# Performance work log

Measured on AMD Instinct MI355X. Metric: run time of the kernel, lower is better.

The kernel has to match this reference:

```python
import jax, jax.numpy as jnp
import numpy as np

N = 50000   # num_nodes
E = 640000  # num_edges (avg degree ~12.8)
D = 128     # input_dim
H = 128     # hidden_dim
T = 100     # targets per head


def setup_inputs() -> dict:
    key = jax.random.key(0)
    ks = jax.random.split(key, 20)
    w = lambda k, s: jax.random.normal(k, s, jnp.float32) * 0.02
    return {
        "x": jax.random.normal(ks[0], (N, D), jnp.float32),
        "edge_index": jax.random.randint(ks[1], (2, E), 0, N, dtype=jnp.int32),
        "edge_weight": jax.random.uniform(ks[2], (E,), jnp.float32),
        "ace_idx": jax.random.randint(ks[3], (T,), 0, N, dtype=jnp.int32),
        "h2_idx": jax.random.randint(ks[4], (T,), 0, N, dtype=jnp.int32),
        "W1": w(ks[5], (D, H)), "b1": jnp.zeros((H,), jnp.float32),
        "W2": w(ks[6], (H, H)), "b2": jnp.zeros((H,), jnp.float32),
        "W3": w(ks[7], (H, H)), "b3": jnp.zeros((H,), jnp.float32),
        "Wh": w(ks[8], (H, H)), "bh": jnp.zeros((H,), jnp.float32),
        "Wace": w(ks[9], (H, 1)), "bace": jnp.zeros((1,), jnp.float32),
        "Wh2": w(ks[10], (H, 1)), "bh2": jnp.zeros((1,), jnp.float32),
    }


def gcn_conv(x, src, dst, ew, W, b):
    # PyG GCNConv: add self-loops (weight 1), symmetric D^-1/2 (A+I) D^-1/2, then XW + b
    n = x.shape[0]
    xw = x @ W                                             # [N, H]
    deg = jax.ops.segment_sum(ew, dst, num_segments=n) + 1.0  # +1 from self-loop
    dinv = jax.lax.rsqrt(jnp.maximum(deg, 1e-12))          # deg >= 1 here
    norm = dinv[src] * ew * dinv[dst]                      # per-edge coefficient
    agg = jax.ops.segment_sum(norm[:, None] * xw[src], dst, num_segments=n)
    agg = agg + (dinv * dinv)[:, None] * xw                # self-loop contribution
    return agg + b


def reference(x, edge_index, edge_weight, ace_idx, h2_idx,
              W1, b1, W2, b2, W3, b3, Wh, bh, Wace, bace, Wh2, bh2):
    src, dst = edge_index[0], edge_index[1]
    h = jax.nn.relu(gcn_conv(x, src, dst, edge_weight, W1, b1))
    h = jax.nn.relu(gcn_conv(h, src, dst, edge_weight, W2, b2))
    h = jax.nn.relu(gcn_conv(h, src, dst, edge_weight, W3, b3))
    # dropout is identity in eval mode
    h = jax.nn.relu(h @ Wh + bh)
    ace_pred = h[ace_idx] @ Wace + bace   # [T, 1]
    h2_pred = h[h2_idx] @ Wh2 + bh2       # [T, 1]
    return jnp.concatenate([ace_pred, h2_pred], axis=0)  # [2T, 1]
```

## Files before the change

### kernel.cpp

```cpp
#include <hip/hip_runtime.h>
#include <math.h>

constexpr int N = 50000;
constexpr int E = 640000;
constexpr int D = 128;
constexpr int T = 100;
constexpr int MAXDEG = 64;
constexpr float SC = 256.0f;
constexpr float SCINV = 1.0f / 256.0f;
constexpr int GB = (N + 127) / 128;
constexpr int EBLK = (E + 255) / 256;
constexpr int ZB = N * 8 / 16 / 256 + 1;
constexpr int WCB = 3 * 16384 / 256;

typedef __attribute__((ext_vector_type(8))) _Float16 half8v;
typedef __attribute__((ext_vector_type(8))) unsigned short ushort8v;
typedef __attribute__((ext_vector_type(4))) float f32x4;

__device__ inline float dinv_of(unsigned int degY) {
  return 1.0f / sqrtf((float)degY * (1.0f / 16777216.0f) + 1.0f);
}


__global__ __launch_bounds__(256) void init_kernel(
    const float* __restrict__ W1, const float* __restrict__ W2,
    const float* __restrict__ W3, uint4* __restrict__ degcnt_v,
    unsigned short* __restrict__ wt0, unsigned short* __restrict__ wt1,
    unsigned short* __restrict__ w3kn) {
  int b = blockIdx.x, tid = threadIdx.x;
  if (b < ZB) {
    int i = b * 256 + tid;
    if (i < N * 8 / 16) degcnt_v[i] = uint4{0, 0, 0, 0};
  } else {
    int idx = (b - ZB) * 256 + tid;
    int layer = idx >> 14;
    int r = idx & 16383;
    if (layer == 0) {
      int n = r >> 7, k = r & 127;
      _Float16 h = (_Float16)(W1[k * D + n] * SC);
      wt0[n * D + k] = *(unsigned short*)&h;
    } else if (layer == 1) {
      int n = r >> 7, k = r & 127;
      _Float16 h = (_Float16)W2[k * D + n];
      wt1[n * D + k] = *(unsigned short*)&h;
    } else {
      int k = r >> 7, n = r & 127;
      _Float16 h = (_Float16)W3[k * D + n];
      w3kn[k * D + n] = *(unsigned short*)&h;
    }
  }
}


__global__ void edge_pass_kernel(const float* __restrict__ ew, const int* __restrict__ src,
                                 const int* __restrict__ dst,
                                 unsigned long long* __restrict__ degcnt,
                                 unsigned int* __restrict__ slot) {
  int e = blockIdx.x * 256 + threadIdx.x;
  if (e < E) {
    float w = ew[e];
    int d = dst[e];
    unsigned int fxdeg = __float2uint_rn(w * 16777216.0f);
    unsigned int fx16 = __float2uint_rn(w * 65536.0f);
    if (fx16 > 65535u) fx16 = 65535u;
    unsigned long long old = atomicAdd(&degcnt[d],
                                       ((unsigned long long)fxdeg << 32) | 1ull);
    unsigned int rank = (unsigned int)(old & 0xffffffffull);
    if (rank < MAXDEG)
      slot[(size_t)d * MAXDEG + rank] = (fx16 << 16) | (unsigned int)src[e];
  }
}


template <bool F32A, bool DINV>
__global__ __launch_bounds__(256) void gemm_nolds_kernel(
    const void* __restrict__ Ain, const unsigned short* __restrict__ Bt,
    const uint2* __restrict__ degcnt, unsigned short* __restrict__ out) {
  const int tid = threadIdx.x;
  const int w = tid >> 6, lane = tid & 63;
  const int q = lane >> 4, n16 = lane & 15;
  const int rbase = w * 32;
  const int row0 = blockIdx.x * 128;

  size_t arow[2];
#pragma unroll
  for (int rt = 0; rt < 2; ++rt) {
    int gr = row0 + rbase + rt * 16 + n16;
    if (gr >= N) gr = N - 1;
    arow[rt] = (size_t)gr * D;
  }
  half8v a[4][2];
#pragma unroll
  for (int kc = 0; kc < 4; ++kc) {
    const int ko = kc * 32 + q * 8;
#pragma unroll
    for (int rt = 0; rt < 2; ++rt) {
      if (F32A) {
        const float* A = (const float*)Ain;
        float4 v0 = *(const float4*)&A[arow[rt] + ko];
        float4 v1 = *(const float4*)&A[arow[rt] + ko + 4];
        half8v h;
        h[0] = (_Float16)v0.x; h[1] = (_Float16)v0.y;
        h[2] = (_Float16)v0.z; h[3] = (_Float16)v0.w;
        h[4] = (_Float16)v1.x; h[5] = (_Float16)v1.y;
        h[6] = (_Float16)v1.z; h[7] = (_Float16)v1.w;
        a[kc][rt] = h;
      } else {
        const unsigned short* A = (const unsigned short*)Ain;
        a[kc][rt] = *(const half8v*)&A[arow[rt] + ko];
      }
    }
  }

  f32x4 acc[2][8] = {};
#pragma unroll
  for (int kc = 0; kc < 4; ++kc) {
    const int ko = kc * 32 + q * 8;
#pragma unroll
    for (int ct = 0; ct < 8; ++ct) {
      int n = ct * 16 + n16;
      half8v b = *(const half8v*)&Bt[n * D + ko];
#pragma unroll
      for (int rt = 0; rt < 2; ++rt) {
        acc[rt][ct] = __builtin_amdgcn_mfma_f32_16x16x32_f16(a[kc][rt], b, acc[rt][ct], 0, 0, 0);
      }
    }
  }

#pragma unroll
  for (int rt = 0; rt < 2; ++rt) {
#pragma unroll
    for (int r = 0; r < 4; ++r) {
      int gr = row0 + rbase + rt * 16 + q * 4 + r;
      if (gr < N) {
        float dv = 1.0f;
        if (DINV) dv = dinv_of(degcnt[gr].y);
#pragma unroll
        for (int ct = 0; ct < 8; ++ct) {
          int col = ct * 16 + n16;
          _Float16 h = (_Float16)(DINV ? acc[rt][ct][r] * dv : acc[rt][ct][r]);
          out[(size_t)gr * D + col] = *(unsigned short*)&h;
        }
      }
    }
  }
}


__global__ __launch_bounds__(256) void agg_kernel(
    const unsigned short* __restrict__ z, const unsigned int* __restrict__ slot,
    const uint2* __restrict__ degcnt, const float* __restrict__ bias,
    unsigned short* __restrict__ oP) {
  int g = (blockIdx.x * 256 + threadIdx.x) >> 4;
  int lane = threadIdx.x & 15;
  const unsigned int* degY = (const unsigned int*)degcnt;

  uint2 pg = degcnt[g];
  int cnt = (int)pg.x; if (cnt > MAXDEG) cnt = MAXDEG;
  float dvg = dinv_of(pg.y);
  half8v xv = *(const half8v*)&z[(size_t)g * D + lane * 8];
  float acc[8];
#pragma unroll
  for (int i = 0; i < 8; ++i) acc[i] = dvg * (float)xv[i];

  const unsigned int* sl = slot + (size_t)g * MAXDEG;
  int k = 0;
  for (; k + 4 <= cnt; k += 4) {
    uint4 p = *(const uint4*)&sl[k];
    float d0 = dinv_of(degY[((p.x & 0xffffu) << 1) + 1]);
    float d1 = dinv_of(degY[((p.y & 0xffffu) << 1) + 1]);
    float d2 = dinv_of(degY[((p.z & 0xffffu) << 1) + 1]);
    float d3 = dinv_of(degY[((p.w & 0xffffu) << 1) + 1]);
    float c0 = (float)(p.x >> 16) * (1.0f / 65536.0f) * d0;
    float c1 = (float)(p.y >> 16) * (1.0f / 65536.0f) * d1;
    float c2 = (float)(p.z >> 16) * (1.0f / 65536.0f) * d2;
    float c3 = (float)(p.w >> 16) * (1.0f / 65536.0f) * d3;
    half8v v0 = *(const half8v*)&z[(size_t)(p.x & 0xffffu) * D + lane * 8];
    half8v v1 = *(const half8v*)&z[(size_t)(p.y & 0xffffu) * D + lane * 8];
    half8v v2 = *(const half8v*)&z[(size_t)(p.z & 0xffffu) * D + lane * 8];
    half8v v3 = *(const half8v*)&z[(size_t)(p.w & 0xffffu) * D + lane * 8];
#pragma unroll
    for (int i = 0; i < 8; ++i) {
      acc[i] = fmaf(c0, (float)v0[i], acc[i]);
      acc[i] = fmaf(c1, (float)v1[i], acc[i]);
      acc[i] = fmaf(c2, (float)v2[i], acc[i]);
      acc[i] = fmaf(c3, (float)v3[i], acc[i]);
    }
  }
  for (; k < cnt; ++k) {
    unsigned int p = sl[k];
    float dsv = dinv_of(degY[((p & 0xffffu) << 1) + 1]);
    float c = (float)(p >> 16) * (1.0f / 65536.0f) * dsv;
    half8v v = *(const half8v*)&z[(size_t)(p & 0xffffu) * D + lane * 8];
#pragma unroll
    for (int i = 0; i < 8; ++i) acc[i] = fmaf(c, (float)v[i], acc[i]);
  }

  half8v hv;
#pragma unroll
  for (int i = 0; i < 8; ++i)
    hv[i] = (_Float16)fmaxf(fmaf(dvg, acc[i], bias[lane * 8 + i] * SC), 0.f);
  *(half8v*)&oP[(size_t)g * D + lane * 8] = hv;
}


__global__ __launch_bounds__(256) void l23_heads_kernel(
    const unsigned short* __restrict__ z2, const unsigned int* __restrict__ slot,
    const uint2* __restrict__ degcnt,
    const float* __restrict__ b2, const float* __restrict__ b3,
    const unsigned short* __restrict__ w3kn,
    const float* __restrict__ Wh, const float* __restrict__ bh,
    const int* __restrict__ ace_idx, const int* __restrict__ h2_idx,
    const float* __restrict__ Wace, const float* __restrict__ bace,
    const float* __restrict__ Wh2, const float* __restrict__ bh2,
    float* __restrict__ out) {
  __shared__ float sacc[16][128];
  __shared__ unsigned short w3l[16384];
  __shared__ float svec[128];
  __shared__ float h3v[128];
  __shared__ float psum[2];
  int t = blockIdx.x;
  int tid = threadIdx.x;
  int node; const float* whead; float bhead;
  if (t < T) { node = ace_idx[t];     whead = Wace; bhead = bace[0]; }
  else       { node = h2_idx[t - T];  whead = Wh2;  bhead = bh2[0]; }

#pragma unroll
  for (int it = 0; it < 8; ++it) {
    int idx = tid + it * 256;
    *(ushort8v*)&w3l[idx * 8] = *(const ushort8v*)&w3kn[idx * 8];
  }

  int grp = tid >> 4, lane = tid & 15;
  float b2l[8];
#pragma unroll
  for (int i = 0; i < 8; ++i) b2l[i] = b2[lane * 8 + i] * SC;

  uint2 pn = degcnt[node];
  int tcnt = (int)pn.x; if (tcnt > MAXDEG) tcnt = MAXDEG;
  float dvn = dinv_of(pn.y);
  const unsigned int* tsl = slot + (size_t)node * MAXDEG;
  int nitems = 1 + tcnt;
  float a[8] = {};
  for (int it = grp; it < nitems; it += 16) {
    int u; float wgt;
    if (it == 0) { u = node; wgt = 1.0f; }
    else {
      unsigned int p = tsl[it - 1];
      wgt = (float)(p >> 16) * (1.0f / 65536.0f);
      u = (int)(p & 0xffffu);
    }
    uint2 pu = degcnt[u];
    float dvu = dinv_of(pu.y);
    int cu = (int)pu.x; if (cu > MAXDEG) cu = MAXDEG;
    half8v xv = *(const half8v*)&z2[(size_t)u * D + lane * 8];
    float r[8];
#pragma unroll
    for (int i = 0; i < 8; ++i) r[i] = (float)xv[i];
    const unsigned int* usl = slot + (size_t)u * MAXDEG;
    int e = 0;
    for (; e + 4 <= cu; e += 4) {
      uint4 p4 = *(const uint4*)&usl[e];
      float c0 = (float)(p4.x >> 16) * (1.0f / 65536.0f);
      float c1 = (float)(p4.y >> 16) * (1.0f / 65536.0f);
      float c2 = (float)(p4.z >> 16) * (1.0f / 65536.0f);
      float c3 = (float)(p4.w >> 16) * (1.0f / 65536.0f);
      half8v v0 = *(const half8v*)&z2[(size_t)(p4.x & 0xffffu) * D + lane * 8];
      half8v v1 = *(const half8v*)&z2[(size_t)(p4.y & 0xffffu) * D + lane * 8];
      half8v v2 = *(const half8v*)&z2[(size_t)(p4.z & 0xffffu) * D + lane * 8];
      half8v v3 = *(const half8v*)&z2[(size_t)(p4.w & 0xffffu) * D + lane * 8];
#pragma unroll
      for (int i = 0; i < 8; ++i) {
        r[i] = fmaf(c0, (float)v0[i], r[i]);
        r[i] = fmaf(c1, (float)v1[i], r[i]);
        r[i] = fmaf(c2, (float)v2[i], r[i]);
        r[i] = fmaf(c3, (float)v3[i], r[i]);
      }
    }
    for (; e < cu; ++e) {
      unsigned int p2 = usl[e];
      float c2 = (float)(p2 >> 16) * (1.0f / 65536.0f);
      half8v v = *(const half8v*)&z2[(size_t)(p2 & 0xffffu) * D + lane * 8];
#pragma unroll
      for (int i = 0; i < 8; ++i) r[i] = fmaf(c2, (float)v[i], r[i]);
    }
#pragma unroll
    for (int i = 0; i < 8; ++i) {
      float h2 = fmaxf(fmaf(dvu, r[i], b2l[i]), 0.f);
      a[i] = fmaf(wgt, dvu * h2, a[i]);
    }
  }
#pragma unroll
  for (int i = 0; i < 8; ++i) sacc[grp][lane * 8 + i] = a[i];
  __syncthreads();

  if (tid < 128) {
    float s = 0.f;
#pragma unroll
    for (int gp = 0; gp < 16; ++gp) s += sacc[gp][tid];
    svec[tid] = s * dvn;
  }
  __syncthreads();

  if (tid < 128) {
    float y = b3[tid] * SC;
#pragma unroll 16
    for (int k = 0; k < 128; ++k) {
      _Float16 wv = *(const _Float16*)&w3l[k * D + tid];
      y = fmaf(svec[k], (float)wv, y);
    }
    h3v[tid] = fmaxf(y, 0.f) * SCINV;
  }
  __syncthreads();

  float v = 0.f;
  if (tid < 128) {
    float acc = bh[tid];
#pragma unroll 16
    for (int k = 0; k < 128; ++k)
      acc = fmaf(h3v[k], Wh[k * D + tid], acc);
    v = fmaxf(acc, 0.f) * whead[tid];
  }
#pragma unroll
  for (int off = 32; off; off >>= 1) v += __shfl_down(v, off, 64);
  if (tid < 128 && (tid & 63) == 0) psum[tid >> 6] = v;
  __syncthreads();
  if (tid == 0) out[t] = psum[0] + psum[1] + bhead;
}


extern "C" void kernel_launch(void* const* d_in, const int* in_sizes, int n_in,
                              void* d_out, int out_size, void* d_ws, size_t ws_size,
                              hipStream_t stream) {
  const float* x    = (const float*)d_in[0];
  const int*   ei   = (const int*)d_in[1];
  const float* ew   = (const float*)d_in[2];
  const int*   ace  = (const int*)d_in[3];
  const int*   h2   = (const int*)d_in[4];
  const float* W1 = (const float*)d_in[5];  const float* b1 = (const float*)d_in[6];
  const float* W2 = (const float*)d_in[7];  const float* b2 = (const float*)d_in[8];
  const float* W3 = (const float*)d_in[9];  const float* b3 = (const float*)d_in[10];
  const float* Wh = (const float*)d_in[11]; const float* bh = (const float*)d_in[12];
  const float* Wace = (const float*)d_in[13]; const float* bace = (const float*)d_in[14];
  const float* Wh2  = (const float*)d_in[15]; const float* bh2  = (const float*)d_in[16];
  const int* src = ei;
  const int* dst = ei + E;

  char* w = (char*)d_ws;
  unsigned long long* degcnt = (unsigned long long*)w;  w += (size_t)N * 8;
  unsigned int* slot = (unsigned int*)w;  w += (size_t)N * MAXDEG * 4;
  unsigned short* wt0 = (unsigned short*)w;  w += 16384 * 2;
  unsigned short* wt1 = (unsigned short*)w;  w += 16384 * 2;
  unsigned short* w3kn = (unsigned short*)w; w += 16384 * 2;
  unsigned short* zbuf = (unsigned short*)w; w += (size_t)N * D * 2;
  unsigned short* P1  = (unsigned short*)w;  w += (size_t)N * D * 2;

  const int AG = N * 16 / 256;

  init_kernel<<<ZB + WCB, 256, 0, stream>>>(W1, W2, W3, (uint4*)degcnt, wt0, wt1, w3kn);
  edge_pass_kernel<<<EBLK, 256, 0, stream>>>(ew, src, dst, degcnt, slot);
  gemm_nolds_kernel<true, false><<<GB, 256, 0, stream>>>(x, wt0, nullptr, zbuf);
  agg_kernel<<<AG, 256, 0, stream>>>(zbuf, slot, (const uint2*)degcnt, b1, P1);
  gemm_nolds_kernel<false, true><<<GB, 256, 0, stream>>>(P1, wt1, (const uint2*)degcnt, zbuf);
  l23_heads_kernel<<<2 * T, 256, 0, stream>>>(zbuf, slot, (const uint2*)degcnt,
                                              b2, b3, w3kn, Wh, bh, ace, h2,
                                              Wace, bace, Wh2, bh2, (float*)d_out);
}
```

Baseline: 216.6 us.

## Fuse edge pass with layer-1 GEMM and split target aggregation across blocks

The edge scatter pass and the first GEMM (x@W1), which are independent, now run in one launch, with different blocks taking different roles, so the two overlap and one launch is saved. The edge pass now handles 4 edges per thread. The layer-2/3 head work is split into a partial kernel with 4 blocks per target (800 blocks instead of 200) that writes partial sums to a workspace buffer, plus a finish kernel that reduces them and applies W3 and the heads. This adds one launch and a small buffer in exchange for more parallelism in the latency-bound target stage.

```diff
diff --git a/kernel.cpp b/kernel.cpp
--- a/kernel.cpp
+++ b/kernel.cpp
@@ -9,7 +9,8 @@
 constexpr float SC = 256.0f;
 constexpr float SCINV = 1.0f / 256.0f;
 constexpr int GB = (N + 127) / 128;
-constexpr int EBLK = (E + 255) / 256;
+constexpr int ESL = E / 4;
+constexpr int EB4 = ESL / 256;
 constexpr int ZB = N * 8 / 16 / 256 + 1;
 constexpr int WCB = 3 * 16384 / 256;
 
@@ -52,29 +53,99 @@
 }
 
 
-__global__ void edge_pass_kernel(const float* __restrict__ ew, const int* __restrict__ src,
-                                 const int* __restrict__ dst,
-                                 unsigned long long* __restrict__ degcnt,
-                                 unsigned int* __restrict__ slot) {
-  int e = blockIdx.x * 256 + threadIdx.x;
-  if (e < E) {
-    float w = ew[e];
-    int d = dst[e];
-    unsigned int fxdeg = __float2uint_rn(w * 16777216.0f);
-    unsigned int fx16 = __float2uint_rn(w * 65536.0f);
-    if (fx16 > 65535u) fx16 = 65535u;
-    unsigned long long old = atomicAdd(&degcnt[d],
-                                       ((unsigned long long)fxdeg << 32) | 1ull);
-    unsigned int rank = (unsigned int)(old & 0xffffffffull);
-    if (rank < MAXDEG)
-      slot[(size_t)d * MAXDEG + rank] = (fx16 << 16) | (unsigned int)src[e];
-  }
-}
-
-
-template <bool F32A, bool DINV>
-__global__ __launch_bounds__(256) void gemm_nolds_kernel(
-    const void* __restrict__ Ain, const unsigned short* __restrict__ Bt,
+__global__ __launch_bounds__(256) void fused_eg1_kernel(
+    const float* __restrict__ ew, const int* __restrict__ src,
+    const int* __restrict__ dst,
+    unsigned long long* __restrict__ degcnt, unsigned int* __restrict__ slot,
+    const float* __restrict__ x, const unsigned short* __restrict__ Bt,
+    unsigned short* __restrict__ z1) {
+  const int b = blockIdx.x;
+  const int tid = threadIdx.x;
+  if (b < EB4) {
+    int gid = b * 256 + tid;
+    float w0 = ew[gid + 0 * ESL], w1 = ew[gid + 1 * ESL];
+    float w2 = ew[gid + 2 * ESL], w3 = ew[gid + 3 * ESL];
+    int d0 = dst[gid + 0 * ESL], d1 = dst[gid + 1 * ESL];
+    int d2 = dst[gid + 2 * ESL], d3 = dst[gid + 3 * ESL];
+    int s0 = src[gid + 0 * ESL], s1 = src[gid + 1 * ESL];
+    int s2 = src[gid + 2 * ESL], s3 = src[gid + 3 * ESL];
+#pragma unroll
+    for (int j = 0; j < 4; ++j) {
+      float w = j == 0 ? w0 : j == 1 ? w1 : j == 2 ? w2 : w3;
+      int d   = j == 0 ? d0 : j == 1 ? d1 : j == 2 ? d2 : d3;
+      int s   = j == 0 ? s0 : j == 1 ? s1 : j == 2 ? s2 : s3;
+      unsigned int fxdeg = __float2uint_rn(w * 16777216.0f);
+      unsigned int fx16 = __float2uint_rn(w * 65536.0f);
+      if (fx16 > 65535u) fx16 = 65535u;
+      unsigned long long old = atomicAdd(&degcnt[d],
+                                         ((unsigned long long)fxdeg << 32) | 1ull);
+      unsigned int rank = (unsigned int)(old & 0xffffffffull);
+      if (rank < MAXDEG)
+        slot[(size_t)d * MAXDEG + rank] = (fx16 << 16) | (unsigned int)s;
+    }
+  } else {
+    const int w = tid >> 6, lane = tid & 63;
+    const int q = lane >> 4, n16 = lane & 15;
+    const int rbase = w * 32;
+    const int row0 = (b - EB4) * 128;
+    size_t arow[2];
+#pragma unroll
+    for (int rt = 0; rt < 2; ++rt) {
+      int gr = row0 + rbase + rt * 16 + n16;
+      if (gr >= N) gr = N - 1;
+      arow[rt] = (size_t)gr * D;
+    }
+    half8v a[4][2];
+#pragma unroll
+    for (int kc = 0; kc < 4; ++kc) {
+      const int ko = kc * 32 + q * 8;
+#pragma unroll
+      for (int rt = 0; rt < 2; ++rt) {
+        float4 v0 = *(const float4*)&x[arow[rt] + ko];
+        float4 v1 = *(const float4*)&x[arow[rt] + ko + 4];
+        half8v h;
+        h[0] = (_Float16)v0.x; h[1] = (_Float16)v0.y;
+        h[2] = (_Float16)v0.z; h[3] = (_Float16)v0.w;
+        h[4] = (_Float16)v1.x; h[5] = (_Float16)v1.y;
+        h[6] = (_Float16)v1.z; h[7] = (_Float16)v1.w;
+        a[kc][rt] = h;
+      }
+    }
+    f32x4 acc[2][8] = {};
+#pragma unroll
+    for (int kc = 0; kc < 4; ++kc) {
+      const int ko = kc * 32 + q * 8;
+#pragma unroll
+      for (int ct = 0; ct < 8; ++ct) {
+        int n = ct * 16 + n16;
+        half8v bb = *(const half8v*)&Bt[n * D + ko];
+#pragma unroll
+        for (int rt = 0; rt < 2; ++rt) {
+          acc[rt][ct] = __builtin_amdgcn_mfma_f32_16x16x32_f16(a[kc][rt], bb, acc[rt][ct], 0, 0, 0);
+        }
+      }
+    }
+#pragma unroll
+    for (int rt = 0; rt < 2; ++rt) {
+#pragma unroll
+      for (int r = 0; r < 4; ++r) {
+        int gr = row0 + rbase + rt * 16 + q * 4 + r;
+        if (gr < N) {
+#pragma unroll
+          for (int ct = 0; ct < 8; ++ct) {
+            int col = ct * 16 + n16;
+            _Float16 h = (_Float16)acc[rt][ct][r];
+            z1[(size_t)gr * D + col] = *(unsigned short*)&h;
+          }
+        }
+      }
+    }
+  }
+}
+
+
+__global__ __launch_bounds__(256) void gemm2_kernel(
+    const unsigned short* __restrict__ A, const unsigned short* __restrict__ Bt,
     const uint2* __restrict__ degcnt, unsigned short* __restrict__ out) {
   const int tid = threadIdx.x;
   const int w = tid >> 6, lane = tid & 63;
@@ -94,24 +165,9 @@
   for (int kc = 0; kc < 4; ++kc) {
     const int ko = kc * 32 + q * 8;
 #pragma unroll
-    for (int rt = 0; rt < 2; ++rt) {
-      if (F32A) {
-        const float* A = (const float*)Ain;
-        float4 v0 = *(const float4*)&A[arow[rt] + ko];
-        float4 v1 = *(const float4*)&A[arow[rt] + ko + 4];
-        half8v h;
-        h[0] = (_Float16)v0.x; h[1] = (_Float16)v0.y;
-        h[2] = (_Float16)v0.z; h[3] = (_Float16)v0.w;
-        h[4] = (_Float16)v1.x; h[5] = (_Float16)v1.y;
-        h[6] = (_Float16)v1.z; h[7] = (_Float16)v1.w;
-        a[kc][rt] = h;
-      } else {
-        const unsigned short* A = (const unsigned short*)Ain;
-        a[kc][rt] = *(const half8v*)&A[arow[rt] + ko];
-      }
-    }
-  }
-
+    for (int rt = 0; rt < 2; ++rt)
+      a[kc][rt] = *(const half8v*)&A[arow[rt] + ko];
+  }
   f32x4 acc[2][8] = {};
 #pragma unroll
   for (int kc = 0; kc < 4; ++kc) {
@@ -126,19 +182,17 @@
       }
     }
   }
-
 #pragma unroll
   for (int rt = 0; rt < 2; ++rt) {
 #pragma unroll
     for (int r = 0; r < 4; ++r) {
       int gr = row0 + rbase + rt * 16 + q * 4 + r;
       if (gr < N) {
-        float dv = 1.0f;
-        if (DINV) dv = dinv_of(degcnt[gr].y);
+        float dv = dinv_of(degcnt[gr].y);
 #pragma unroll
         for (int ct = 0; ct < 8; ++ct) {
           int col = ct * 16 + n16;
-          _Float16 h = (_Float16)(DINV ? acc[rt][ct][r] * dv : acc[rt][ct][r]);
+          _Float16 h = (_Float16)(acc[rt][ct][r] * dv);
           out[(size_t)gr * D + col] = *(unsigned short*)&h;
         }
       }
@@ -204,51 +258,35 @@
 }
 
 
-__global__ __launch_bounds__(256) void l23_heads_kernel(
+__global__ __launch_bounds__(256) void l23_part_kernel(
     const unsigned short* __restrict__ z2, const unsigned int* __restrict__ slot,
-    const uint2* __restrict__ degcnt,
-    const float* __restrict__ b2, const float* __restrict__ b3,
-    const unsigned short* __restrict__ w3kn,
-    const float* __restrict__ Wh, const float* __restrict__ bh,
+    const uint2* __restrict__ degcnt, const float* __restrict__ b2,
     const int* __restrict__ ace_idx, const int* __restrict__ h2_idx,
-    const float* __restrict__ Wace, const float* __restrict__ bace,
-    const float* __restrict__ Wh2, const float* __restrict__ bh2,
-    float* __restrict__ out) {
+    float* __restrict__ pacc) {
   __shared__ float sacc[16][128];
-  __shared__ unsigned short w3l[16384];
-  __shared__ float svec[128];
-  __shared__ float h3v[128];
-  __shared__ float psum[2];
-  int t = blockIdx.x;
+  int b = blockIdx.x;
+  int t = b >> 2, p = b & 3;
   int tid = threadIdx.x;
-  int node; const float* whead; float bhead;
-  if (t < T) { node = ace_idx[t];     whead = Wace; bhead = bace[0]; }
-  else       { node = h2_idx[t - T];  whead = Wh2;  bhead = bh2[0]; }
-
-#pragma unroll
-  for (int it = 0; it < 8; ++it) {
-    int idx = tid + it * 256;
-    *(ushort8v*)&w3l[idx * 8] = *(const ushort8v*)&w3kn[idx * 8];
-  }
+  int node = (t < T) ? ace_idx[t] : h2_idx[t - T];
 
   int grp = tid >> 4, lane = tid & 15;
+  int G = p * 16 + grp;
   float b2l[8];
 #pragma unroll
   for (int i = 0; i < 8; ++i) b2l[i] = b2[lane * 8 + i] * SC;
 
   uint2 pn = degcnt[node];
   int tcnt = (int)pn.x; if (tcnt > MAXDEG) tcnt = MAXDEG;
-  float dvn = dinv_of(pn.y);
   const unsigned int* tsl = slot + (size_t)node * MAXDEG;
   int nitems = 1 + tcnt;
   float a[8] = {};
-  for (int it = grp; it < nitems; it += 16) {
+  for (int it = G; it < nitems; it += 64) {
     int u; float wgt;
     if (it == 0) { u = node; wgt = 1.0f; }
     else {
-      unsigned int p = tsl[it - 1];
-      wgt = (float)(p >> 16) * (1.0f / 65536.0f);
-      u = (int)(p & 0xffffu);
+      unsigned int pk = tsl[it - 1];
+      wgt = (float)(pk >> 16) * (1.0f / 65536.0f);
+      u = (int)(pk & 0xffffu);
     }
     uint2 pu = degcnt[u];
     float dvu = dinv_of(pu.y);
@@ -298,7 +336,38 @@
     float s = 0.f;
 #pragma unroll
     for (int gp = 0; gp < 16; ++gp) s += sacc[gp][tid];
-    svec[tid] = s * dvn;
+    pacc[(size_t)(t * 4 + p) * 128 + tid] = s;
+  }
+}
+
+
+__global__ __launch_bounds__(256) void l23_finish_kernel(
+    const uint2* __restrict__ degcnt, const float* __restrict__ pacc,
+    const float* __restrict__ b3, const unsigned short* __restrict__ w3kn,
+    const float* __restrict__ Wh, const float* __restrict__ bh,
+    const int* __restrict__ ace_idx, const int* __restrict__ h2_idx,
+    const float* __restrict__ Wace, const float* __restrict__ bace,
+    const float* __restrict__ Wh2, const float* __restrict__ bh2,
+    float* __restrict__ out) {
+  __shared__ unsigned short w3l[16384];
+  __shared__ float svec[128];
+  __shared__ float h3v[128];
+  __shared__ float psum[2];
+  int t = blockIdx.x;
+  int tid = threadIdx.x;
+  int node; const float* whead; float bhead;
+  if (t < T) { node = ace_idx[t];     whead = Wace; bhead = bace[0]; }
+  else       { node = h2_idx[t - T];  whead = Wh2;  bhead = bh2[0]; }
+
+#pragma unroll
+  for (int it = 0; it < 8; ++it) {
+    int idx = tid + it * 256;
+    *(ushort8v*)&w3l[idx * 8] = *(const ushort8v*)&w3kn[idx * 8];
+  }
+  if (tid < 128) {
+    const float* pa = &pacc[(size_t)t * 4 * 128];
+    float s = pa[tid] + pa[128 + tid] + pa[256 + tid] + pa[384 + tid];
+    svec[tid] = s * dinv_of(degcnt[node].y);
   }
   __syncthreads();
 
@@ -352,17 +421,19 @@
   unsigned short* wt0 = (unsigned short*)w;  w += 16384 * 2;
   unsigned short* wt1 = (unsigned short*)w;  w += 16384 * 2;
   unsigned short* w3kn = (unsigned short*)w; w += 16384 * 2;
+  float* pacc = (float*)w;                   w += (size_t)2 * T * 4 * 128 * 4;
   unsigned short* zbuf = (unsigned short*)w; w += (size_t)N * D * 2;
   unsigned short* P1  = (unsigned short*)w;  w += (size_t)N * D * 2;
 
   const int AG = N * 16 / 256;
 
   init_kernel<<<ZB + WCB, 256, 0, stream>>>(W1, W2, W3, (uint4*)degcnt, wt0, wt1, w3kn);
-  edge_pass_kernel<<<EBLK, 256, 0, stream>>>(ew, src, dst, degcnt, slot);
-  gemm_nolds_kernel<true, false><<<GB, 256, 0, stream>>>(x, wt0, nullptr, zbuf);
+  fused_eg1_kernel<<<EB4 + GB, 256, 0, stream>>>(ew, src, dst, degcnt, slot, x, wt0, zbuf);
   agg_kernel<<<AG, 256, 0, stream>>>(zbuf, slot, (const uint2*)degcnt, b1, P1);
-  gemm_nolds_kernel<false, true><<<GB, 256, 0, stream>>>(P1, wt1, (const uint2*)degcnt, zbuf);
-  l23_heads_kernel<<<2 * T, 256, 0, stream>>>(zbuf, slot, (const uint2*)degcnt,
-                                              b2, b3, w3kn, Wh, bh, ace, h2,
-                                              Wace, bace, Wh2, bh2, (float*)d_out);
-}
+  gemm2_kernel<<<GB, 256, 0, stream>>>(P1, wt1, (const uint2*)degcnt, zbuf);
+  l23_part_kernel<<<4 * 2 * T, 256, 0, stream>>>(zbuf, slot, (const uint2*)degcnt,
+                                                 b2, ace, h2, pacc);
+  l23_finish_kernel<<<2 * T, 256, 0, stream>>>((const uint2*)degcnt, pacc, b3, w3kn,
+                                               Wh, bh, ace, h2,
+                                               Wace, bace, Wh2, bh2, (float*)d_out);
+}
```

Result: no change. 212.4 us (-1.9%).
